# Kernel tuning notes

Hardware: AMD Instinct MI355X
Metric: run time of the kernel (lower is better)

The kernel has to match this reference:

```python
import jax, jax.numpy as jnp
import numpy as np

B, O, M, H, E = 32, 64, 128, 4, 64  # batch, num_obj, memory_len, heads, embed


def setup_inputs() -> dict:
    key = jax.random.key(0)
    ks = jax.random.split(key, 10)
    s = 1.0 / np.sqrt(E)
    return {
        "query": jax.random.normal(ks[0], (B, O, E), jnp.float32),
        "context": jax.random.normal(ks[1], (B, M, E), jnp.float32),
        "memory": jax.random.normal(ks[2], (B, M, E), jnp.float32),
        "W_ch": jax.random.normal(ks[3], (E, H * E), jnp.float32) * s,
        "b_ch": jax.random.normal(ks[4], (H * E,), jnp.float32) * s,
        "w_logit": jax.random.normal(ks[5], (E,), jnp.float32) * s,
        "b_logit": jax.random.normal(ks[6], (1,), jnp.float32) * s,
        "W_rh": jax.random.normal(ks[7], (H * E, E), jnp.float32) * (1.0 / np.sqrt(H * E)),
        "b_rh": jax.random.normal(ks[8], (E,), jnp.float32) * (1.0 / np.sqrt(H * E)),
        "temp": jnp.float32(1.0),
    }


def reference(query, context, memory, W_ch, b_ch, w_logit, b_logit, W_rh, b_rh, temp):
    # create heads: [B,O,E] -> [B,O,H,E]
    q = (query @ W_ch + b_ch).reshape(B, O, H, E)
    # broadcast add query heads and context over memory axis: [B,O,M,H,E]
    qc = jnp.tanh(context[:, None, :, None, :] + q[:, :, None, :, :])
    # logit projection -> [B,O,M,H]
    logits = jnp.einsum("bomhe,e->bomh", qc, w_logit) + b_logit[0]
    # softmax over memory axis (dim=2)
    probs = jax.nn.softmax(logits / temp, axis=2)
    # weighted sum of memory over M: [B,O,H,E]
    heads = jnp.einsum("bomh,bme->bohe", probs, memory)
    heads = jax.nn.leaky_relu(heads, negative_slope=0.01)
    out = heads.reshape(B, O, H * E) @ W_rh + b_rh
    return out
```

## Files before the change

### kernel.cpp

```cpp
#include <hip/hip_runtime.h>
#include <hip/hip_fp16.h>

#define B 32
#define O 64
#define M 128
#define H 4
#define E 64
#define SC 2.88539008177792681f
#define LOG2E 1.44269504088896341f

#if __has_builtin(__builtin_amdgcn_exp2f)
#define EXP2F(x) __builtin_amdgcn_exp2f(x)
#else
#define EXP2F(x) __exp2f(x)
#endif

__device__ __forceinline__ float rl(float v, int lane) {
    return __uint_as_float(__builtin_amdgcn_readlane(__float_as_uint(v), lane));
}

__global__ __launch_bounds__(256) void attn_fused(
    const float* __restrict__ query, const float* __restrict__ context,
    const float* __restrict__ memory, const float* __restrict__ W_ch,
    const float* __restrict__ b_ch, const float* __restrict__ w_logit,
    const float* __restrict__ b_logit, const float* __restrict__ temp,
    const float* __restrict__ W_rh, const float* __restrict__ b_rh,
    float* __restrict__ out)
{
    __shared__ __half2 s_E[E * 64];
    __shared__ float2 s_q2[E];
    __shared__ float4 s_qwu[H * E];
    __shared__ float  s_prob0[M * H];
    __shared__ float  s_prob1[M * H];
    __shared__ float  s_part0[H * 4 * E];
    __shared__ float  s_part1[H * 4 * E];
    __shared__ float  s_po0[4 * E];
    __shared__ float  s_po1[4 * E];

    const int t = threadIdx.x, lane = t & 63, w = t >> 6;
    const int bo0 = blockIdx.x * 2, bo1 = bo0 + 1, b = bo0 >> 6;

    if (t < 128)
        ((float*)s_q2)[t] = query[(size_t)(bo0 + (t & 1)) * E + (t >> 1)];
    const float wl  = w_logit[lane];
    const float bl  = b_logit[0];
    const float lsc = LOG2E / temp[0];
    float a0 = b_ch[t];
    float a1 = a0;
    __syncthreads();

    {
        const float* Wp = W_ch + t;
        #pragma unroll 8
        for (int k = 0; k < 64; ++k) {
            float wv = Wp[k * 256];
            float2 qv = s_q2[k];
            a0 = fmaf(qv.x, wv, a0);
            a1 = fmaf(qv.y, wv, a1);
        }
    }
    s_qwu[t] = make_float4(wl, EXP2F(SC * a0), EXP2F(SC * a1), 0.f);

    {
        const float* cp = context + (size_t)b * (M * E) + lane;
        #pragma unroll 4
        for (int p = 0; p < 16; ++p) {
            int c = p * 4 + w;
            float f0 = cp[(2 * c) * 64];
            float f1 = cp[(2 * c) * 64 + 64];
            float ea = fminf(EXP2F(SC * f0), 60000.f);
            float eb = fminf(EXP2F(SC * f1), 60000.f);
            s_E[lane * 64 + (c ^ lane)] =
                __halves2half2(__float2half_rn(ea), __float2half_rn(eb));
        }
    }

    float sumw = wl;
    #pragma unroll
    for (int sft = 1; sft < 64; sft <<= 1) sumw += __shfl_xor(sumw, sft);
    const float base = (sumw + bl) * lsc;
    const float lsc2 = -2.0f * lsc;
    __syncthreads();

    float a00 = 0.f, a01 = 0.f, a10 = 0.f, a11 = 0.f;
    const float4* qp = &s_qwu[w * 64];
    #pragma unroll 4
    for (int e = 0; e < 64; ++e) {
        float2 cf = __half22float2(s_E[e * 64 + (lane ^ e)]);
        float4 qw = qp[e];
        float t00 = fmaf(cf.x, qw.y, 1.0f);
        float t01 = fmaf(cf.y, qw.y, 1.0f);
        float t10 = fmaf(cf.x, qw.z, 1.0f);
        float t11 = fmaf(cf.y, qw.z, 1.0f);
        float r0 = __builtin_amdgcn_rcpf(t00 * t01);
        float r1 = __builtin_amdgcn_rcpf(t10 * t11);
        float w0 = qw.x * r0;
        float w1 = qw.x * r1;
        a00 = fmaf(w0, t01, a00);  a01 = fmaf(w0, t00, a01);
        a10 = fmaf(w1, t11, a10);  a11 = fmaf(w1, t10, a11);
    }

    float mrx[16], mry[16];
    {
        const float* mp = memory + (size_t)b * (M * E) + (32 * w) * 64 + lane;
        #pragma unroll
        for (int j = 0; j < 16; ++j) {
            mrx[j] = mp[(2 * j) * 64];
            mry[j] = mp[(2 * j) * 64 + 64];
        }
    }

    float l00 = fmaf(lsc2, a00, base), l01 = fmaf(lsc2, a01, base);
    float l10 = fmaf(lsc2, a10, base), l11 = fmaf(lsc2, a11, base);
    float mx0 = fmaxf(l00, l01), mx1 = fmaxf(l10, l11);
    #pragma unroll
    for (int sft = 1; sft < 64; sft <<= 1) {
        mx0 = fmaxf(mx0, __shfl_xor(mx0, sft));
        mx1 = fmaxf(mx1, __shfl_xor(mx1, sft));
    }
    float e00 = EXP2F(l00 - mx0), e01 = EXP2F(l01 - mx0);
    float e10 = EXP2F(l10 - mx1), e11 = EXP2F(l11 - mx1);
    float s0 = e00 + e01, s1 = e10 + e11;
    #pragma unroll
    for (int sft = 1; sft < 64; sft <<= 1) {
        s0 += __shfl_xor(s0, sft);
        s1 += __shfl_xor(s1, sft);
    }
    float rs0 = __builtin_amdgcn_rcpf(s0), rs1 = __builtin_amdgcn_rcpf(s1);
    s_prob0[(2 * lane) * H + w]     = e00 * rs0;
    s_prob0[(2 * lane + 1) * H + w] = e01 * rs0;
    s_prob1[(2 * lane) * H + w]     = e10 * rs1;
    s_prob1[(2 * lane + 1) * H + w] = e11 * rs1;
    __syncthreads();

    float h00 = 0.f, h01 = 0.f, h02 = 0.f, h03 = 0.f;
    float h10 = 0.f, h11 = 0.f, h12 = 0.f, h13 = 0.f;
    {
        const int mbase = 32 * w;
        #pragma unroll 8
        for (int j = 0; j < 16; ++j) {
            float mvx = mrx[j], mvy = mry[j];
            int m = mbase + 2 * j;
            float4 pa = *(const float4*)(&s_prob0[m * 4]);
            float4 pb = *(const float4*)(&s_prob0[(m + 1) * 4]);
            h00 = fmaf(pa.x, mvx, h00); h01 = fmaf(pa.y, mvx, h01);
            h02 = fmaf(pa.z, mvx, h02); h03 = fmaf(pa.w, mvx, h03);
            h00 = fmaf(pb.x, mvy, h00); h01 = fmaf(pb.y, mvy, h01);
            h02 = fmaf(pb.z, mvy, h02); h03 = fmaf(pb.w, mvy, h03);
            float4 pc = *(const float4*)(&s_prob1[m * 4]);
            float4 pd = *(const float4*)(&s_prob1[(m + 1) * 4]);
            h10 = fmaf(pc.x, mvx, h10); h11 = fmaf(pc.y, mvx, h11);
            h12 = fmaf(pc.z, mvx, h12); h13 = fmaf(pc.w, mvx, h13);
            h10 = fmaf(pd.x, mvy, h10); h11 = fmaf(pd.y, mvy, h11);
            h12 = fmaf(pd.z, mvy, h12); h13 = fmaf(pd.w, mvy, h13);
        }
    }
    s_part0[0 * 256 + w * 64 + lane] = h00;
    s_part0[1 * 256 + w * 64 + lane] = h01;
    s_part0[2 * 256 + w * 64 + lane] = h02;
    s_part0[3 * 256 + w * 64 + lane] = h03;
    s_part1[0 * 256 + w * 64 + lane] = h10;
    s_part1[1 * 256 + w * 64 + lane] = h11;
    s_part1[2 * 256 + w * 64 + lane] = h12;
    s_part1[3 * 256 + w * 64 + lane] = h13;
    __syncthreads();
    float hv0 = s_part0[w * 256 + lane] + s_part0[w * 256 + 64 + lane]
              + s_part0[w * 256 + 128 + lane] + s_part0[w * 256 + 192 + lane];
    float hv1 = s_part1[w * 256 + lane] + s_part1[w * 256 + 64 + lane]
              + s_part1[w * 256 + 128 + lane] + s_part1[w * 256 + 192 + lane];
    hv0 = (hv0 > 0.f) ? hv0 : 0.01f * hv0;
    hv1 = (hv1 > 0.f) ? hv1 : 0.01f * hv1;

    {
        float acc0 = 0.f, acc1 = 0.f;
        const float* Wp = W_rh + (w * 64) * 64 + lane;
        #pragma unroll 8
        for (int jj = 0; jj < 64; ++jj) {
            float wv = Wp[jj * 64];
            float hj0 = rl(hv0, jj);
            float hj1 = rl(hv1, jj);
            acc0 = fmaf(hj0, wv, acc0);
            acc1 = fmaf(hj1, wv, acc1);
        }
        s_po0[w * 64 + lane] = acc0;
        s_po1[w * 64 + lane] = acc1;
    }
    __syncthreads();
    if (t < 64) {
        float o = s_po0[t] + s_po0[64 + t] + s_po0[128 + t] + s_po0[192 + t] + b_rh[t];
        out[(size_t)bo0 * 64 + t] = o;
    } else if (t < 128) {
        int e2 = t - 64;
        float o = s_po1[e2] + s_po1[64 + e2] + s_po1[128 + e2] + s_po1[192 + e2] + b_rh[e2];
        out[(size_t)bo1 * 64 + e2] = o;
    }
}

extern "C" void kernel_launch(void* const* d_in, const int* in_sizes, int n_in,
                              void* d_out, int out_size, void* d_ws, size_t ws_size,
                              hipStream_t stream) {
    const float* query   = (const float*)d_in[0];
    const float* context = (const float*)d_in[1];
    const float* memory  = (const float*)d_in[2];
    const float* W_ch    = (const float*)d_in[3];
    const float* b_ch    = (const float*)d_in[4];
    const float* w_logit = (const float*)d_in[5];
    const float* b_logit = (const float*)d_in[6];
    const float* W_rh    = (const float*)d_in[7];
    const float* b_rh    = (const float*)d_in[8];
    const float* temp    = (const float*)d_in[9];
    float* out = (float*)d_out;

    attn_fused<<<B * O / 2, 256, 0, stream>>>(query, context, memory, W_ch, b_ch,
                                              w_logit, b_logit, temp, W_rh, b_rh, out);
}
```

Baseline: 92.00 us.

## Prefetch W_ch in register batches, share one reciprocal, use LDS for output GEMV

Loads the first 16 rows of W_ch into registers before the context exp stage. The rest of the query projection is software-pipelined in 16-row batches after the barrier, which overlaps global-load latency with other work. The tanh-derivative loop now uses one reciprocal for both query rows instead of two, at the cost of extra multiplies and some precision and overflow risk from the larger product. The output projection reads hidden values as float4 from LDS instead of using readlane, reusing the prob buffers, which relies on the earlier barrier ordering.

```diff
diff --git a/kernel.cpp b/kernel.cpp
--- a/kernel.cpp
+++ b/kernel.cpp
@@ -14,10 +14,6 @@
 #else
 #define EXP2F(x) __exp2f(x)
 #endif
-
-__device__ __forceinline__ float rl(float v, int lane) {
-    return __uint_as_float(__builtin_amdgcn_readlane(__float_as_uint(v), lane));
-}
 
 __global__ __launch_bounds__(256) void attn_fused(
     const float* __restrict__ query, const float* __restrict__ context,
@@ -47,19 +43,11 @@
     const float lsc = LOG2E / temp[0];
     float a0 = b_ch[t];
     float a1 = a0;
-    __syncthreads();
-
-    {
-        const float* Wp = W_ch + t;
-        #pragma unroll 8
-        for (int k = 0; k < 64; ++k) {
-            float wv = Wp[k * 256];
-            float2 qv = s_q2[k];
-            a0 = fmaf(qv.x, wv, a0);
-            a1 = fmaf(qv.y, wv, a1);
-        }
-    }
-    s_qwu[t] = make_float4(wl, EXP2F(SC * a0), EXP2F(SC * a1), 0.f);
+
+    const float* Wp = W_ch + t;
+    float wb0[16], wb1[16];
+    #pragma unroll
+    for (int k = 0; k < 16; ++k) wb0[k] = Wp[k * 256];
 
     {
         const float* cp = context + (size_t)b * (M * E) + lane;
@@ -82,6 +70,39 @@
     const float lsc2 = -2.0f * lsc;
     __syncthreads();
 
+    #pragma unroll
+    for (int k = 0; k < 16; ++k) wb1[k] = Wp[(16 + k) * 256];
+    #pragma unroll
+    for (int k = 0; k < 16; ++k) {
+        float2 qv = s_q2[k];
+        a0 = fmaf(qv.x, wb0[k], a0);
+        a1 = fmaf(qv.y, wb0[k], a1);
+    }
+    #pragma unroll
+    for (int k = 0; k < 16; ++k) wb0[k] = Wp[(32 + k) * 256];
+    #pragma unroll
+    for (int k = 0; k < 16; ++k) {
+        float2 qv = s_q2[16 + k];
+        a0 = fmaf(qv.x, wb1[k], a0);
+        a1 = fmaf(qv.y, wb1[k], a1);
+    }
+    #pragma unroll
+    for (int k = 0; k < 16; ++k) wb1[k] = Wp[(48 + k) * 256];
+    #pragma unroll
+    for (int k = 0; k < 16; ++k) {
+        float2 qv = s_q2[32 + k];
+        a0 = fmaf(qv.x, wb0[k], a0);
+        a1 = fmaf(qv.y, wb0[k], a1);
+    }
+    #pragma unroll
+    for (int k = 0; k < 16; ++k) {
+        float2 qv = s_q2[48 + k];
+        a0 = fmaf(qv.x, wb1[k], a0);
+        a1 = fmaf(qv.y, wb1[k], a1);
+    }
+    s_qwu[t] = make_float4(wl, EXP2F(SC * a0), EXP2F(SC * a1), 0.f);
+    __syncthreads();
+
     float a00 = 0.f, a01 = 0.f, a10 = 0.f, a11 = 0.f;
     const float4* qp = &s_qwu[w * 64];
     #pragma unroll 4
@@ -92,10 +113,12 @@
         float t01 = fmaf(cf.y, qw.y, 1.0f);
         float t10 = fmaf(cf.x, qw.z, 1.0f);
         float t11 = fmaf(cf.y, qw.z, 1.0f);
-        float r0 = __builtin_amdgcn_rcpf(t00 * t01);
-        float r1 = __builtin_amdgcn_rcpf(t10 * t11);
-        float w0 = qw.x * r0;
-        float w1 = qw.x * r1;
+        float p0 = t00 * t01;
+        float p1 = t10 * t11;
+        float r  = __builtin_amdgcn_rcpf(p0 * p1);
+        float wr = qw.x * r;
+        float w0 = wr * p1;
+        float w1 = wr * p0;
         a00 = fmaf(w0, t01, a00);  a01 = fmaf(w0, t00, a01);
         a10 = fmaf(w1, t11, a10);  a11 = fmaf(w1, t10, a11);
     }
@@ -172,15 +195,26 @@
     hv1 = (hv1 > 0.f) ? hv1 : 0.01f * hv1;
 
     {
+        float* s_hv0 = s_prob0;
+        float* s_hv1 = s_prob1;
+        s_hv0[t] = hv0;
+        s_hv1[t] = hv1;
+        const float4* hq0 = (const float4*)(s_hv0 + w * 64);
+        const float4* hq1 = (const float4*)(s_hv1 + w * 64);
         float acc0 = 0.f, acc1 = 0.f;
-        const float* Wp = W_rh + (w * 64) * 64 + lane;
-        #pragma unroll 8
-        for (int jj = 0; jj < 64; ++jj) {
-            float wv = Wp[jj * 64];
-            float hj0 = rl(hv0, jj);
-            float hj1 = rl(hv1, jj);
-            acc0 = fmaf(hj0, wv, acc0);
-            acc1 = fmaf(hj1, wv, acc1);
+        const float* Wp2 = W_rh + (w * 64) * 64 + lane;
+        #pragma unroll 4
+        for (int q4 = 0; q4 < 16; ++q4) {
+            float4 h0 = hq0[q4];
+            float4 h1 = hq1[q4];
+            float wv0 = Wp2[(4 * q4 + 0) * 64];
+            float wv1 = Wp2[(4 * q4 + 1) * 64];
+            float wv2 = Wp2[(4 * q4 + 2) * 64];
+            float wv3 = Wp2[(4 * q4 + 3) * 64];
+            acc0 = fmaf(h0.x, wv0, acc0);  acc1 = fmaf(h1.x, wv0, acc1);
+            acc0 = fmaf(h0.y, wv1, acc0);  acc1 = fmaf(h1.y, wv1, acc1);
+            acc0 = fmaf(h0.z, wv2, acc0);  acc1 = fmaf(h1.z, wv2, acc1);
+            acc0 = fmaf(h0.w, wv3, acc0);  acc1 = fmaf(h1.w, wv3, acc1);
         }
         s_po0[w * 64 + lane] = acc0;
         s_po1[w * 64 + lane] = acc1;
```

After: 91.21 us. No clear change (-0.9%).
